# Performance work log

Hardware: AMD Instinct MI355X
Metric: run time of the kernel (lower is better)

Reference implementation:

```python
import jax, jax.numpy as jnp
import numpy as np

N = 20000        # atoms
NEIGH = 12       # neighbors per atom
BSTEPS = 40      # bond GBF steps, range [0, 8]
ASTEPS = 20      # angle GBF steps, range [-1, 1]
H = 64           # hidden size
NCLS = 2         # n_classification
NCRYS = 20       # crystals (contiguous blocks of 1000 atoms)
NREL = 3         # edge relation types


def gbf(data, dmin, dmax, steps):
    # Gaussian basis expansion: exp(-(d - mu)^2 / gamma^2), gamma = (max-min)/steps
    filters = jnp.linspace(dmin, dmax, steps)
    gamma = (dmax - dmin) / steps
    return jnp.exp(-((data[..., None] - filters) ** 2) / gamma ** 2)


def rgcn(x, src, dst, etype, W_rel, W_root, b):
    # RGCNConv (PyG default): out = x @ W_root + b + sum_r mean_{j in N_r(i)} x_j @ W_r
    out = x @ W_root + b
    for r in range(NREL):
        w = (etype == r).astype(x.dtype)                     # [E]
        msg = (x @ W_rel[r])[src] * w[:, None]               # transform-then-gather: [E, H]
        s = jax.ops.segment_sum(msg, dst, num_segments=x.shape[0])
        c = jax.ops.segment_sum(w, dst, num_segments=x.shape[0])
        out = out + s / jnp.maximum(c, 1.0)[:, None]
    return out


def _forward(bond_fea, angle_fea, species, nbr_idx, crys_idx,
             W1b_rel, W1b_root, b1b, W1a_rel, W1a_root, b1a,
             W2b_rel, W2b_root, b2b, W2a_rel, W2a_root, b2a,
             fc_W, fc_b):
    n = bond_fea.shape[0]
    src = jnp.repeat(jnp.arange(n, dtype=jnp.int32), NEIGH)  # edge sources
    dst = nbr_idx.reshape(-1)                                # edge targets
    etype = species[src] + species[dst]                      # 0/1/2 per species pair

    edge_fea = gbf(bond_fea, 0.0, 8.0, BSTEPS).reshape(n, -1)      # [N, 480]
    ang_fea = gbf(angle_fea, -1.0, 1.0, ASTEPS).reshape(n, -1)     # [N, 2880]

    bf = jax.nn.relu(rgcn(edge_fea, src, dst, etype, W1b_rel, W1b_root, b1b))
    af = jax.nn.relu(rgcn(ang_fea, src, dst, etype, W1a_rel, W1a_root, b1a))
    # dropout treated as identity (eval/deterministic reference)
    bf = jax.nn.relu(rgcn(bf, src, dst, etype, W2b_rel, W2b_root, b2b))
    af = jax.nn.relu(rgcn(af, src, dst, etype, W2a_rel, W2a_root, b2a))

    feat = jnp.concatenate([bf, af], axis=1)                 # [N, 128]

    # pool: mean over contiguous [start, end) ranges per crystal
    starts = crys_idx[:, 0]
    crys_id = jnp.searchsorted(starts, jnp.arange(n), side='right') - 1
    sums = jax.ops.segment_sum(feat, crys_id, num_segments=NCRYS)
    counts = (crys_idx[:, 1] - crys_idx[:, 0]).astype(feat.dtype)[:, None]
    pooled = sums / counts                                   # [NCRYS, 128]

    return pooled @ fc_W + fc_b                              # [NCRYS, NCLS]


def setup_inputs() -> dict:
    key = jax.random.key(0)
    ks = jax.random.split(key, 20)
    bond_fea = jax.random.uniform(ks[0], (N, NEIGH), dtype=jnp.float32) * 8.0
    angle_fea = jax.random.uniform(ks[1], (N, NEIGH, NEIGH), dtype=jnp.float32) * 2.0 - 1.0
    species = jax.random.randint(ks[2], (N,), 0, 2, dtype=jnp.int32)
    nbr_idx = jax.random.randint(ks[3], (N, NEIGH), 0, N, dtype=jnp.int32)
    starts = jnp.arange(NCRYS, dtype=jnp.int32) * (N // NCRYS)
    crys_idx = jnp.stack([starts, starts + (N // NCRYS)], axis=1)

    def w(k, shape, fan_in):
        return jax.random.normal(k, shape, dtype=jnp.float32) / np.sqrt(fan_in)

    in_b = BSTEPS * NEIGH            # 480
    in_a = ASTEPS * NEIGH * NEIGH    # 2880
    return {
        'bond_fea': bond_fea, 'angle_fea': angle_fea, 'species': species,
        'nbr_idx': nbr_idx, 'crys_idx': crys_idx,
        'W1b_rel': w(ks[4], (NREL, in_b, H), in_b), 'W1b_root': w(ks[5], (in_b, H), in_b),
        'b1b': jnp.zeros((H,), jnp.float32),
        'W1a_rel': w(ks[6], (NREL, in_a, H), in_a), 'W1a_root': w(ks[7], (in_a, H), in_a),
        'b1a': jnp.zeros((H,), jnp.float32),
        'W2b_rel': w(ks[8], (NREL, H, H), H), 'W2b_root': w(ks[9], (H, H), H),
        'b2b': jnp.zeros((H,), jnp.float32),
        'W2a_rel': w(ks[10], (NREL, H, H), H), 'W2a_root': w(ks[11], (H, H), H),
        'b2a': jnp.zeros((H,), jnp.float32),
        'fc_W': w(ks[12], (2 * H, NCLS), 2 * H), 'fc_b': jnp.zeros((NCLS,), jnp.float32),
    }


def reference(bond_fea, angle_fea, species, nbr_idx, crys_idx,
              W1b_rel, W1b_root, b1b, W1a_rel, W1a_root, b1a,
              W2b_rel, W2b_root, b2b, W2a_rel, W2a_root, b2a,
              fc_W, fc_b):
    return _forward(bond_fea, angle_fea, species, nbr_idx, crys_idx,
                    W1b_rel, W1b_root, b1b, W1a_rel, W1a_root, b1a,
                    W2b_rel, W2b_root, b2b, W2a_rel, W2a_root, b2a,
                    fc_W, fc_b)
```

## Files before the change

kernel.cpp:

```cpp
#include <hip/hip_runtime.h>

#define NN 20000
#define NNP 20096
#define NEIGH 12
#define NCRYS 20
#define MT2 1256
#define NSUB 16

typedef __bf16 bf16x8 __attribute__((ext_vector_type(8)));
typedef __bf16 bf16x4 __attribute__((ext_vector_type(4)));
typedef float f32x4 __attribute__((ext_vector_type(4)));
typedef float f32x2 __attribute__((ext_vector_type(2)));

__device__ __forceinline__ void pack_one(const float* Wrel, const float* Wroot,
                                         __bf16* Wp, int K, int idx) {
    int k = idx >> 8, n = idx & 255;
    int r = n >> 6, h = n & 63;
    float v = (r < 3) ? Wrel[((size_t)r * K + k) * 64 + h] : Wroot[(size_t)k * 64 + h];
    int kt = k >> 5, k8 = (k >> 3) & 3, j = k & 7, nt = n >> 4, ni = n & 15;
    Wp[((((size_t)kt * 16 + nt) * 4 + k8) * 16 + ni) * 8 + j] = (__bf16)v;
}

__global__ __launch_bounds__(256) void setup_kernel(
    const int* __restrict__ species, const int* __restrict__ nbr,
    int* __restrict__ adj, int* __restrict__ deg,
    const float* __restrict__ W1b_rel, const float* __restrict__ W1b_root,
    const float* __restrict__ W1a_rel, const float* __restrict__ W1a_root,
    const float* __restrict__ W2b_rel, const float* __restrict__ W2b_root,
    const float* __restrict__ W2a_rel, const float* __restrict__ W2a_root,
    __bf16* __restrict__ Wp1b, __bf16* __restrict__ Wp1a,
    __bf16* __restrict__ Wp2b, __bf16* __restrict__ Wp2a,
    const float* __restrict__ bond, const float* __restrict__ angle,
    float* __restrict__ bondT, float* __restrict__ angleT) {
    __shared__ float ls[64 * 145];
    const int bx = blockIdx.x, tid = threadIdx.x;
    if (bx < 938) {
        int e = bx * 256 + tid;
        if (e < NN * NEIGH) {
            int i = e / NEIGH;
            int d = nbr[e];
            int r = species[i] + species[d];
            int slot = atomicAdd(&deg[d], 1);
            if (slot < 64) adj[(size_t)d * 64 + slot] = i | (r << 28);
        }
    } else if (bx < 938 + 256) {
        const int S0 = 480 * 256, S1 = S0 + 2880 * 256, S2 = S1 + 64 * 256, S3 = S2 + 64 * 256;
        for (int idx = (bx - 938) * 256 + tid; idx < S3; idx += 256 * 256) {
            if (idx < S0)       pack_one(W1b_rel, W1b_root, Wp1b, 480, idx);
            else if (idx < S1)  pack_one(W1a_rel, W1a_root, Wp1a, 2880, idx - S0);
            else if (idx < S2)  pack_one(W2b_rel, W2b_root, Wp2b, 64, idx - S1);
            else                pack_one(W2a_rel, W2a_root, Wp2a, 64, idx - S2);
        }
    } else {
        int tb = bx - 1194;
        if (tb < 314) {
            int m0 = tb * 64;
            for (int idx = tid; idx < 64 * 144; idx += 256) {
                int mm = idx / 144, j = idx - mm * 144;
                int m = m0 + mm;
                ls[mm * 145 + j] = (m < NN) ? angle[(size_t)m * 144 + j] : 0.f;
            }
            __syncthreads();
            for (int idx = tid; idx < 144 * 64; idx += 256) {
                int j = idx >> 6, mm = idx & 63;
                angleT[(size_t)j * NNP + m0 + mm] = ls[mm * 145 + j];
            }
        } else {
            int m0 = (tb - 314) * 64;
            for (int idx = tid; idx < 64 * 12; idx += 256) {
                int mm = idx / 12, j = idx - mm * 12;
                int m = m0 + mm;
                ls[mm * 13 + j] = (m < NN) ? bond[(size_t)m * 12 + j] : 0.f;
            }
            __syncthreads();
            for (int idx = tid; idx < 12 * 64; idx += 256) {
                int j = idx >> 6, mm = idx & 63;
                bondT[(size_t)j * NNP + m0 + mm] = ls[mm * 13 + j];
            }
        }
    }
}

template <int MODE>
__device__ __forceinline__ void gemm1_body(const float* __restrict__ xT,
                                           const __bf16* __restrict__ Wp,
                                           float* __restrict__ Y, int mb,
                                           __bf16* __restrict__ Al) {
    constexpr int KTOT = (MODE == 0) ? 512 : 2880;
    constexpr int NPH = KTOT / 64;
    constexpr int DIVN = (MODE == 0) ? 40 : 20;
    constexpr int ADDJ = 64 / DIVN;
    constexpr int ADDS = 64 % DIVN;
    constexpr float F0 = (MODE == 0) ? 0.f : -1.f;
    constexpr float FS = (MODE == 0) ? (8.f / 39.f) : (2.f / 19.f);
    constexpr float NG2 = ((MODE == 0) ? -25.f : -100.f) * 1.44269504f;
    const float C  = __builtin_amdgcn_exp2f(2.f * NG2 * FS * FS);
    const float P1 = NG2 * FS * FS;
    const float P2 = -2.f * NG2 * FS;

    const int tid = threadIdx.x;
    const int lane = tid & 63, wv = tid >> 6;
    const int m0 = mb * 64;
    const int smt = tid >> 7;
    const int sk8 = (tid >> 5) & 3;
    const int smi = (tid >> 1) & 15;
    const int sjh = (tid & 1) * 4;
    const int sgm = m0 + smt * 16 + smi;
    const int kk0 = sk8 * 8 + sjh;
    const int swoff = (((smt * 4 + sk8) * 16 + smi) * 8 + sjh);
    const int k8b = lane >> 4, nib = lane & 15;
    const bf16x8* Bg = (const bf16x8*)Wp;

    f32x4 acc[4][2] = {};
    bf16x8 bcur[4];

    int jr0 = kk0 / DIVN,        s0 = kk0 % DIVN;
    int jr1 = (32 + kk0) / DIVN, s1 = (32 + kk0) % DIVN;

    auto bload = [&](int ph) {
#pragma unroll
        for (int jf = 0; jf < 4; ++jf)
            bcur[jf] = Bg[(((size_t)(2 * ph + (jf >> 1)) * 16 + 2 * wv + (jf & 1)) * 4 + k8b) * 16 + nib];
    };
    auto advance = [&]() {
        jr0 += ADDJ; s0 += ADDS; if (s0 >= DIVN) { s0 -= DIVN; ++jr0; }
        jr1 += ADDJ; s1 += ADDS; if (s1 >= DIVN) { s1 -= DIVN; ++jr1; }
    };
    auto stage = [&](float a0, float a1, __bf16* dst) {
        f32x2 d;
        d.x = a0 - (F0 + (float)s0 * FS);
        d.y = a1 - (F0 + (float)s1 * FS);
        f32x2 t = d * d;
        f32x2 argE = t * NG2;
        f32x2 argQ = d * P2 + P1;
        f32x2 e0, q0;
        e0.x = __builtin_amdgcn_exp2f(argE.x);
        e0.y = __builtin_amdgcn_exp2f(argE.y);
        q0.x = __builtin_amdgcn_exp2f(argQ.x);
        q0.y = __builtin_amdgcn_exp2f(argQ.y);
        f32x2 e1 = e0 * q0;
        f32x2 q1 = q0 * C;
        f32x2 e2 = e1 * q1;
        f32x2 e3 = e2 * (q1 * C);
        bf16x4 v0, v1;
        v0[0] = (__bf16)e0.x; v0[1] = (__bf16)e1.x; v0[2] = (__bf16)e2.x; v0[3] = (__bf16)e3.x;
        v1[0] = (__bf16)e0.y; v1[1] = (__bf16)e1.y; v1[2] = (__bf16)e2.y; v1[3] = (__bf16)e3.y;
        *(bf16x4*)&dst[swoff] = v0;
        *(bf16x4*)&dst[2048 + swoff] = v1;
    };

    {
        float a0 = xT[(size_t)jr0 * NNP + sgm];
        float a1 = xT[(size_t)jr1 * NNP + sgm];
        stage(a0, a1, Al);
        advance();
    }
    float an0 = xT[(size_t)jr0 * NNP + sgm];
    float an1 = xT[(size_t)jr1 * NNP + sgm];
    bload(0);
    __syncthreads();

    int cur = 0;
    for (int ph = 0; ph < NPH; ++ph) {
        const __bf16* Ab = Al + (cur << 12);
        bf16x8 af[4];
#pragma unroll
        for (int t4 = 0; t4 < 4; ++t4)
            af[t4] = *(const bf16x8*)&Ab[((((t4 << 2) + k8b) << 4) + nib) << 3];
#pragma unroll
        for (int i = 0; i < 4; ++i) {
            acc[i][0] = __builtin_amdgcn_mfma_f32_16x16x32_bf16(af[i], bcur[0], acc[i][0], 0, 0, 0);
            acc[i][1] = __builtin_amdgcn_mfma_f32_16x16x32_bf16(af[i], bcur[1], acc[i][1], 0, 0, 0);
        }
        bf16x8 ag[4];
#pragma unroll
        for (int t4 = 0; t4 < 4; ++t4)
            ag[t4] = *(const bf16x8*)&Ab[2048 + (((((t4 << 2) + k8b) << 4) + nib) << 3)];
#pragma unroll
        for (int i = 0; i < 4; ++i) {
            acc[i][0] = __builtin_amdgcn_mfma_f32_16x16x32_bf16(ag[i], bcur[2], acc[i][0], 0, 0, 0);
            acc[i][1] = __builtin_amdgcn_mfma_f32_16x16x32_bf16(ag[i], bcur[3], acc[i][1], 0, 0, 0);
        }
        if (ph + 1 < NPH) {
            bload(ph + 1);
            stage(an0, an1, Al + ((cur ^ 1) << 12));
            advance();
            if (ph + 2 < NPH) {
                an0 = xT[(size_t)jr0 * NNP + sgm];
                an1 = xT[(size_t)jr1 * NNP + sgm];
            }
        }
        __syncthreads();
        cur ^= 1;
    }

    const int mrow0 = m0 + ((lane >> 4) << 2);
    const int ncol = (wv << 5) + nib;
#pragma unroll
    for (int i = 0; i < 4; ++i)
#pragma unroll
        for (int j = 0; j < 2; ++j)
#pragma unroll
            for (int v = 0; v < 4; ++v) {
                int m = mrow0 + i * 16 + v;
                if (m < NN) Y[(size_t)m * 256 + ncol + j * 16] = acc[i][j][v];
            }
}

__global__ __launch_bounds__(512, 4) void mega_gemm1(const float* __restrict__ bondT,
                                                     const float* __restrict__ angleT,
                                                     const __bf16* __restrict__ Wp1b,
                                                     const __bf16* __restrict__ Wp1a,
                                                     float* __restrict__ Yb, float* __restrict__ Ya) {
    __shared__ __align__(16) __bf16 Al[2 * 4096];
    int bx = blockIdx.x;
    if (bx < 314) gemm1_body<1>(angleT, Wp1a, Ya, bx, Al);
    else          gemm1_body<0>(bondT, Wp1b, Yb, bx - 314, Al);
}

__global__ __launch_bounds__(256) void mega_gemm2(const __bf16* __restrict__ Hbp,
                                                  const __bf16* __restrict__ Hap,
                                                  const __bf16* __restrict__ Wp2b,
                                                  const __bf16* __restrict__ Wp2a,
                                                  float* __restrict__ Yb, float* __restrict__ Ya) {
    __shared__ __align__(16) __bf16 Al[4096];
    __shared__ __align__(16) __bf16 Bl[4096];
    const int ch = blockIdx.x & 1;
    const int mb = blockIdx.x >> 1;
    const int nb = blockIdx.y;
    const __bf16* Ap = ch ? Hap : Hbp;
    const __bf16* Wp = ch ? Wp2a : Wp2b;
    float* Y = ch ? Ya : Yb;
    const int tid = threadIdx.x;
    const int lane = tid & 63, wv = tid >> 6;
    const int m0 = mb * 128;
    const int rw = wv & 1, cw = wv >> 1;
    f32x4 acc[4][4] = {};
#pragma unroll
    for (int kt = 0; kt < 2; ++kt) {
        __syncthreads();
        {
            const float4* src = (const float4*)(Wp + (((size_t)kt * 16 + nb * 8) << 9));
            float4* dst = (float4*)Bl;
            float4 v0 = src[tid], v1 = src[tid + 256];
            dst[tid] = v0;
            dst[tid + 256] = v1;
        }
        {
            const float4* src = (const float4*)(Ap + (((size_t)kt * MT2 + mb * 8) << 9));
            float4* dst = (float4*)Al;
            float4 v0 = src[tid], v1 = src[tid + 256];
            dst[tid] = v0;
            dst[tid + 256] = v1;
        }
        __syncthreads();
        bf16x8 af[4], bfr[4];
        int fro = ((lane >> 4) << 4) + (lane & 15);
#pragma unroll
        for (int t4 = 0; t4 < 4; ++t4) {
            af[t4] = *(const bf16x8*)&Al[((((rw * 4 + t4) << 6) + fro) << 3)];
            bfr[t4] = *(const bf16x8*)&Bl[((((cw * 4 + t4) << 6) + fro) << 3)];
        }
#pragma unroll
        for (int i = 0; i < 4; ++i)
#pragma unroll
            for (int j = 0; j < 4; ++j)
                acc[i][j] = __builtin_amdgcn_mfma_f32_16x16x32_bf16(af[i], bfr[j], acc[i][j], 0, 0, 0);
    }
    const int n0 = nb * 128 + cw * 64;
    const int mrow0 = m0 + rw * 64 + ((lane >> 4) << 2);
    const int ncol = n0 + (lane & 15);
#pragma unroll
    for (int i = 0; i < 4; ++i)
#pragma unroll
        for (int j = 0; j < 4; ++j)
#pragma unroll
            for (int v = 0; v < 4; ++v) {
                int m = mrow0 + i * 16 + v;
                if (m < NN) Y[(size_t)m * 256 + ncol + j * 16] = acc[i][j][v];
            }
}

__device__ __forceinline__ float agg_node(const float* __restrict__ Y,
                                          const int* __restrict__ adj,
                                          const int* __restrict__ deg,
                                          const float* __restrict__ bias,
                                          int node, int h) {
    int dg = min(deg[node], 64);
    int e = adj[(size_t)node * 64 + h];
    bool val = h < dg;
    int r = e >> 28;
    unsigned long long bl0 = __ballot(val && r == 0);
    unsigned long long bl1 = __ballot(val && r == 1);
    unsigned long long bl2 = __ballot(val && r == 2);
    int c0 = __popcll(bl0), c1 = __popcll(bl1), c2 = __popcll(bl2);
    float s0 = 0.f, s1 = 0.f, s2 = 0.f;
    if (dg > 0) {
        int e0 = __builtin_amdgcn_readfirstlane(e);
        int ec = val ? e : e0;
        for (int k0 = 0; k0 < dg; k0 += 16) {
            float v[16];
#pragma unroll
            for (int i = 0; i < 16; ++i) {
                int ek = __builtin_amdgcn_readlane(ec, k0 + i);
                v[i] = Y[(size_t)(ek & 0x0FFFFFFF) * 256 + (ek >> 28) * 64 + h];
            }
#pragma unroll
            for (int i = 0; i < 16; ++i) {
                int kk = k0 + i;
                if (kk < dg) {
                    int rr = __builtin_amdgcn_readlane(ec, kk) >> 28;
                    if (rr == 0) s0 += v[i];
                    else if (rr == 1) s1 += v[i];
                    else s2 += v[i];
                }
            }
        }
    }
    float o = Y[(size_t)node * 256 + 192 + h] + bias[h] +
              s0 / fmaxf((float)c0, 1.f) + s1 / fmaxf((float)c1, 1.f) +
              s2 / fmaxf((float)c2, 1.f);
    return fmaxf(o, 0.f);
}

__global__ __launch_bounds__(256) void agg_packed(const float* __restrict__ Yb,
                                                  const float* __restrict__ Ya,
                                                  const int* __restrict__ adj,
                                                  const int* __restrict__ deg,
                                                  const float* __restrict__ biasb,
                                                  const float* __restrict__ biasa,
                                                  __bf16* __restrict__ outb,
                                                  __bf16* __restrict__ outa) {
    const float* Y = blockIdx.y ? Ya : Yb;
    const float* bias = blockIdx.y ? biasa : biasb;
    __bf16* outp = blockIdx.y ? outa : outb;
    int node = blockIdx.x * 4 + (threadIdx.x >> 6);
    int h = threadIdx.x & 63;
    float o = (node < NN) ? agg_node(Y, adj, deg, bias, node, h) : 0.f;
    int mt = node >> 4, mi = node & 15;
    int ktt = h >> 5, k8 = (h >> 3) & 3, j = h & 7;
    outp[((((size_t)ktt * MT2 + mt) * 4 + k8) * 16 + mi) * 8 + j] = (__bf16)o;
}

__global__ __launch_bounds__(256) void agg_pool(const float* __restrict__ Yb,
                                                const float* __restrict__ Ya,
                                                const int* __restrict__ adj,
                                                const int* __restrict__ deg,
                                                const float* __restrict__ biasb,
                                                const float* __restrict__ biasa,
                                                const int* __restrict__ crys,
                                                float* __restrict__ pooled) {
    const float* Y = blockIdx.y ? Ya : Yb;
    const float* bias = blockIdx.y ? biasa : biasb;
    const int base = blockIdx.y ? 64 : 0;
    int node = blockIdx.x * 4 + (threadIdx.x >> 6);
    int h = threadIdx.x & 63;
    if (node >= NN) return;
    float o = agg_node(Y, adj, deg, bias, node, h);
    int c = 0;
#pragma unroll
    for (int t = 1; t < NCRYS; ++t) c += (node >= crys[t * 2]) ? 1 : 0;
    int sub = blockIdx.x & (NSUB - 1);
    atomicAdd(&pooled[((size_t)c * NSUB + sub) * 128 + base + h], o);
}

__global__ void final2(const float* __restrict__ pooled, const int* __restrict__ crys,
                       const float* __restrict__ fcW, const float* __restrict__ fcb,
                       float* __restrict__ out) {
    int c = blockIdx.x >> 1, o = blockIdx.x & 1;
    int l = threadIdx.x;
    float cnt = (float)(crys[c * 2 + 1] - crys[c * 2]);
    float sb = 0.f, sa = 0.f;
    for (int s = 0; s < NSUB; ++s) {
        sb += pooled[((size_t)c * NSUB + s) * 128 + l];
        sa += pooled[((size_t)c * NSUB + s) * 128 + 64 + l];
    }
    float a = sb * fcW[l * 2 + o] + sa * fcW[(64 + l) * 2 + o];
    for (int s = 32; s > 0; s >>= 1) a += __shfl_down(a, s);
    if (l == 0) out[c * 2 + o] = a / cnt + fcb[o];
}

extern "C" void kernel_launch(void* const* d_in, const int* in_sizes, int n_in,
                              void* d_out, int out_size, void* d_ws, size_t ws_size,
                              hipStream_t stream) {
    const float* bond    = (const float*)d_in[0];
    const float* angle   = (const float*)d_in[1];
    const int*   species = (const int*)d_in[2];
    const int*   nbr     = (const int*)d_in[3];
    const int*   crys    = (const int*)d_in[4];
    const float* W1b_rel = (const float*)d_in[5];
    const float* W1b_root= (const float*)d_in[6];
    const float* b1b     = (const float*)d_in[7];
    const float* W1a_rel = (const float*)d_in[8];
    const float* W1a_root= (const float*)d_in[9];
    const float* b1a     = (const float*)d_in[10];
    const float* W2b_rel = (const float*)d_in[11];
    const float* W2b_root= (const float*)d_in[12];
    const float* b2b     = (const float*)d_in[13];
    const float* W2a_rel = (const float*)d_in[14];
    const float* W2a_root= (const float*)d_in[15];
    const float* b2a     = (const float*)d_in[16];
    const float* fcW     = (const float*)d_in[17];
    const float* fcb     = (const float*)d_in[18];
    float* out = (float*)d_out;

    char* ws = (char*)d_ws;
    size_t off = 0;
    auto alloc = [&](size_t bytes) {
        char* p = ws + off;
        off = (off + bytes + 255) & ~(size_t)255;
        return p;
    };
    __bf16* Wp1b = (__bf16*)alloc((size_t)512 * 256 * 2);
    __bf16* Wp1a = (__bf16*)alloc((size_t)2880 * 256 * 2);
    __bf16* Wp2b = (__bf16*)alloc((size_t)64 * 256 * 2);
    __bf16* Wp2a = (__bf16*)alloc((size_t)64 * 256 * 2);
    float*  bondT = (float*)alloc((size_t)16 * NNP * 4);
    float*  angleT= (float*)alloc((size_t)144 * NNP * 4);
    float*  Yb   = (float*)alloc((size_t)NN * 256 * 4);
    float*  Ya   = (float*)alloc((size_t)NN * 256 * 4);
    __bf16* Hbp  = (__bf16*)alloc((size_t)2 * MT2 * 512 * 2);
    __bf16* Hap  = (__bf16*)alloc((size_t)2 * MT2 * 512 * 2);
    int*    adj  = (int*)alloc((size_t)NN * 64 * 4);
    int*    deg  = (int*)alloc((size_t)NN * 4);
    float*  pooled = (float*)alloc((size_t)NCRYS * NSUB * 128 * 4);

    hipMemsetAsync(deg, 0, (size_t)NN * 4, stream);
    hipMemsetAsync(pooled, 0, (size_t)NCRYS * NSUB * 128 * 4, stream);
    hipMemsetAsync(Wp1b, 0, (size_t)512 * 256 * 2, stream);
    hipMemsetAsync(bondT, 0, (size_t)16 * NNP * 4, stream);

    setup_kernel<<<1822, 256, 0, stream>>>(species, nbr, adj, deg,
                                           W1b_rel, W1b_root, W1a_rel, W1a_root,
                                           W2b_rel, W2b_root, W2a_rel, W2a_root,
                                           Wp1b, Wp1a, Wp2b, Wp2a,
                                           bond, angle, bondT, angleT);

    mega_gemm1<<<628, 512, 0, stream>>>(bondT, angleT, Wp1b, Wp1a, Yb, Ya);
    agg_packed<<<dim3(5024, 2), 256, 0, stream>>>(Yb, Ya, adj, deg, b1b, b1a, Hbp, Hap);
    mega_gemm2<<<dim3(314, 2), 256, 0, stream>>>(Hbp, Hap, Wp2b, Wp2a, Yb, Ya);
    agg_pool<<<dim3(5000, 2), 256, 0, stream>>>(Yb, Ya, adj, deg, b2b, b2a, crys, pooled);
    final2<<<NCRYS * 2, 64, 0, stream>>>(pooled, crys, fcW, fcb, out);
}
```

Before: 261.1 us.

## Aggregate-then-transform for layer two using bf16 features and concatenated weights

```diff
diff --git a/kernel.cpp b/kernel.cpp
--- a/kernel.cpp
+++ b/kernel.cpp
@@ -10,7 +10,6 @@
 typedef __bf16 bf16x8 __attribute__((ext_vector_type(8)));
 typedef __bf16 bf16x4 __attribute__((ext_vector_type(4)));
 typedef float f32x4 __attribute__((ext_vector_type(4)));
-typedef float f32x2 __attribute__((ext_vector_type(2)));
 
 __device__ __forceinline__ void pack_one(const float* Wrel, const float* Wroot,
                                          __bf16* Wp, int K, int idx) {
@@ -19,6 +18,15 @@
     float v = (r < 3) ? Wrel[((size_t)r * K + k) * 64 + h] : Wroot[(size_t)k * 64 + h];
     int kt = k >> 5, k8 = (k >> 3) & 3, j = k & 7, nt = n >> 4, ni = n & 15;
     Wp[((((size_t)kt * 16 + nt) * 4 + k8) * 16 + ni) * 8 + j] = (__bf16)v;
+}
+
+__device__ __forceinline__ void pack_cat(const float* Wrel, const float* Wroot,
+                                         __bf16* Wp, int idx) {
+    int k4 = idx >> 6, n = idx & 63;
+    int q = k4 >> 6, kk = k4 & 63;
+    float v = q ? Wrel[(((q - 1) * 64 + kk) * 64) + n] : Wroot[kk * 64 + n];
+    int kt = k4 >> 5, k8 = (k4 >> 3) & 3, j = k4 & 7, nt = n >> 4, ni = n & 15;
+    Wp[((((size_t)kt * 4 + nt) * 4 + k8) * 16 + ni) * 8 + j] = (__bf16)v;
 }
 
 __global__ __launch_bounds__(256) void setup_kernel(
@@ -44,12 +52,12 @@
             if (slot < 64) adj[(size_t)d * 64 + slot] = i | (r << 28);
         }
     } else if (bx < 938 + 256) {
-        const int S0 = 480 * 256, S1 = S0 + 2880 * 256, S2 = S1 + 64 * 256, S3 = S2 + 64 * 256;
+        const int S0 = 480 * 256, S1 = S0 + 2880 * 256, S2 = S1 + 16384, S3 = S2 + 16384;
         for (int idx = (bx - 938) * 256 + tid; idx < S3; idx += 256 * 256) {
             if (idx < S0)       pack_one(W1b_rel, W1b_root, Wp1b, 480, idx);
             else if (idx < S1)  pack_one(W1a_rel, W1a_root, Wp1a, 2880, idx - S0);
-            else if (idx < S2)  pack_one(W2b_rel, W2b_root, Wp2b, 64, idx - S1);
-            else                pack_one(W2a_rel, W2a_root, Wp2a, 64, idx - S2);
+            else if (idx < S2)  pack_cat(W2b_rel, W2b_root, Wp2b, idx - S1);
+            else                pack_cat(W2a_rel, W2a_root, Wp2a, idx - S2);
         }
     } else {
         int tb = bx - 1194;
@@ -86,7 +94,7 @@
                                            const __bf16* __restrict__ Wp,
                                            float* __restrict__ Y, int mb,
                                            __bf16* __restrict__ Al) {
-    constexpr int KTOT = (MODE == 0) ? 512 : 2880;
+    constexpr int KTOT = (MODE == 0) ? 512 : 2944;
     constexpr int NPH = KTOT / 64;
     constexpr int DIVN = (MODE == 0) ? 40 : 20;
     constexpr int ADDJ = 64 / DIVN;
@@ -109,89 +117,90 @@
     const int kk0 = sk8 * 8 + sjh;
     const int swoff = (((smt * 4 + sk8) * 16 + smi) * 8 + sjh);
     const int k8b = lane >> 4, nib = lane & 15;
-    const bf16x8* Bg = (const bf16x8*)Wp;
 
     f32x4 acc[4][2] = {};
-    bf16x8 bcur[4];
-
-    int jr0 = kk0 / DIVN,        s0 = kk0 % DIVN;
-    int jr1 = (32 + kk0) / DIVN, s1 = (32 + kk0) % DIVN;
-
-    auto bload = [&](int ph) {
-#pragma unroll
-        for (int jf = 0; jf < 4; ++jf)
-            bcur[jf] = Bg[(((size_t)(2 * ph + (jf >> 1)) * 16 + 2 * wv + (jf & 1)) * 4 + k8b) * 16 + nib];
-    };
-    auto advance = [&]() {
-        jr0 += ADDJ; s0 += ADDS; if (s0 >= DIVN) { s0 -= DIVN; ++jr0; }
-        jr1 += ADDJ; s1 += ADDS; if (s1 >= DIVN) { s1 -= DIVN; ++jr1; }
+
+    const float* pA0 = xT + (size_t)(kk0 / DIVN) * NNP + sgm;
+    const float* pA1 = xT + (size_t)((32 + kk0) / DIVN) * NNP + sgm;
+    int sL0 = kk0 % DIVN, sL1 = (32 + kk0) % DIVN;
+    int sS0 = sL0, sS1 = sL1;
+
+    const bf16x8* pB0 = (const bf16x8*)Wp + ((size_t)(2 * wv) * 4 + k8b) * 16 + nib;
+    const bf16x8* pB1 = pB0 + 1024;
+
+    bf16x8 bEv[4], bOd[4];
+
+    auto advL = [&]() {
+        sL0 += ADDS;
+        if (sL0 >= DIVN) { sL0 -= DIVN; pA0 += (size_t)(ADDJ + 1) * NNP; } else pA0 += (size_t)ADDJ * NNP;
+        sL1 += ADDS;
+        if (sL1 >= DIVN) { sL1 -= DIVN; pA1 += (size_t)(ADDJ + 1) * NNP; } else pA1 += (size_t)ADDJ * NNP;
+    };
+    auto advS = [&]() {
+        sS0 += ADDS; if (sS0 >= DIVN) sS0 -= DIVN;
+        sS1 += ADDS; if (sS1 >= DIVN) sS1 -= DIVN;
+    };
+    auto loadB = [&](bf16x8* d) {
+        d[0] = pB0[0]; d[1] = pB0[64]; d[2] = pB1[0]; d[3] = pB1[64];
+        pB0 += 2048; pB1 += 2048;
     };
     auto stage = [&](float a0, float a1, __bf16* dst) {
-        f32x2 d;
-        d.x = a0 - (F0 + (float)s0 * FS);
-        d.y = a1 - (F0 + (float)s1 * FS);
-        f32x2 t = d * d;
-        f32x2 argE = t * NG2;
-        f32x2 argQ = d * P2 + P1;
-        f32x2 e0, q0;
-        e0.x = __builtin_amdgcn_exp2f(argE.x);
-        e0.y = __builtin_amdgcn_exp2f(argE.y);
-        q0.x = __builtin_amdgcn_exp2f(argQ.x);
-        q0.y = __builtin_amdgcn_exp2f(argQ.y);
-        f32x2 e1 = e0 * q0;
-        f32x2 q1 = q0 * C;
-        f32x2 e2 = e1 * q1;
-        f32x2 e3 = e2 * (q1 * C);
+        float d0 = a0 - (F0 + (float)sS0 * FS);
+        float d1 = a1 - (F0 + (float)sS1 * FS);
+        float e0a = __builtin_amdgcn_exp2f(NG2 * d0 * d0);
+        float q0a = __builtin_amdgcn_exp2f(fmaf(P2, d0, P1));
+        float e0b = __builtin_amdgcn_exp2f(NG2 * d1 * d1);
+        float q0b = __builtin_amdgcn_exp2f(fmaf(P2, d1, P1));
+        float e1a = e0a * q0a, q1a = q0a * C;
+        float e2a = e1a * q1a, e3a = e2a * q1a * C;
+        float e1b = e0b * q0b, q1b = q0b * C;
+        float e2b = e1b * q1b, e3b = e2b * q1b * C;
         bf16x4 v0, v1;
-        v0[0] = (__bf16)e0.x; v0[1] = (__bf16)e1.x; v0[2] = (__bf16)e2.x; v0[3] = (__bf16)e3.x;
-        v1[0] = (__bf16)e0.y; v1[1] = (__bf16)e1.y; v1[2] = (__bf16)e2.y; v1[3] = (__bf16)e3.y;
+        v0[0] = (__bf16)e0a; v0[1] = (__bf16)e1a; v0[2] = (__bf16)e2a; v0[3] = (__bf16)e3a;
+        v1[0] = (__bf16)e0b; v1[1] = (__bf16)e1b; v1[2] = (__bf16)e2b; v1[3] = (__bf16)e3b;
         *(bf16x4*)&dst[swoff] = v0;
         *(bf16x4*)&dst[2048 + swoff] = v1;
     };
-
-    {
-        float a0 = xT[(size_t)jr0 * NNP + sgm];
-        float a1 = xT[(size_t)jr1 * NNP + sgm];
-        stage(a0, a1, Al);
-        advance();
-    }
-    float an0 = xT[(size_t)jr0 * NNP + sgm];
-    float an1 = xT[(size_t)jr1 * NNP + sgm];
-    bload(0);
+    auto mma = [&](const __bf16* Ab, const bf16x8* bc) {
+        bf16x8 af[4], ag[4];
+#pragma unroll
+        for (int t4 = 0; t4 < 4; ++t4) {
+            af[t4] = *(const bf16x8*)&Ab[(((((t4 << 2) + k8b) << 4) + nib) << 3)];
+            ag[t4] = *(const bf16x8*)&Ab[2048 + (((((t4 << 2) + k8b) << 4) + nib) << 3)];
+        }
+#pragma unroll
+        for (int i = 0; i < 4; ++i) {
+            acc[i][0] = __builtin_amdgcn_mfma_f32_16x16x32_bf16(af[i], bc[0], acc[i][0], 0, 0, 0);
+            acc[i][1] = __builtin_amdgcn_mfma_f32_16x16x32_bf16(af[i], bc[1], acc[i][1], 0, 0, 0);
+        }
+#pragma unroll
+        for (int i = 0; i < 4; ++i) {
+            acc[i][0] = __builtin_amdgcn_mfma_f32_16x16x32_bf16(ag[i], bc[2], acc[i][0], 0, 0, 0);
+            acc[i][1] = __builtin_amdgcn_mfma_f32_16x16x32_bf16(ag[i], bc[3], acc[i][1], 0, 0, 0);
+        }
+    };
+
+    float a00 = pA0[0], a01 = pA1[0]; advL();
+    float aN0 = pA0[0], aN1 = pA1[0]; advL();
+    stage(a00, a01, Al); advS();
+    loadB(bEv);
+    loadB(bOd);
     __syncthreads();
 
-    int cur = 0;
-    for (int ph = 0; ph < NPH; ++ph) {
-        const __bf16* Ab = Al + (cur << 12);
-        bf16x8 af[4];
-#pragma unroll
-        for (int t4 = 0; t4 < 4; ++t4)
-            af[t4] = *(const bf16x8*)&Ab[((((t4 << 2) + k8b) << 4) + nib) << 3];
-#pragma unroll
-        for (int i = 0; i < 4; ++i) {
-            acc[i][0] = __builtin_amdgcn_mfma_f32_16x16x32_bf16(af[i], bcur[0], acc[i][0], 0, 0, 0);
-            acc[i][1] = __builtin_amdgcn_mfma_f32_16x16x32_bf16(af[i], bcur[1], acc[i][1], 0, 0, 0);
-        }
-        bf16x8 ag[4];
-#pragma unroll
-        for (int t4 = 0; t4 < 4; ++t4)
-            ag[t4] = *(const bf16x8*)&Ab[2048 + (((((t4 << 2) + k8b) << 4) + nib) << 3)];
-#pragma unroll
-        for (int i = 0; i < 4; ++i) {
-            acc[i][0] = __builtin_amdgcn_mfma_f32_16x16x32_bf16(ag[i], bcur[2], acc[i][0], 0, 0, 0);
-            acc[i][1] = __builtin_amdgcn_mfma_f32_16x16x32_bf16(ag[i], bcur[3], acc[i][1], 0, 0, 0);
-        }
-        if (ph + 1 < NPH) {
-            bload(ph + 1);
-            stage(an0, an1, Al + ((cur ^ 1) << 12));
-            advance();
-            if (ph + 2 < NPH) {
-                an0 = xT[(size_t)jr0 * NNP + sgm];
-                an1 = xT[(size_t)jr1 * NNP + sgm];
-            }
-        }
+    for (int p2 = 0; p2 < NPH / 2; ++p2) {
+        const bool last = (p2 == NPH / 2 - 1);
+        mma(Al, bEv);
+        if (!last) loadB(bEv);
+        stage(aN0, aN1, Al + 4096); advS();
+        if (!last) { aN0 = pA0[0]; aN1 = pA1[0]; advL(); }
         __syncthreads();
-        cur ^= 1;
+        mma(Al + 4096, bOd);
+        if (!last) {
+            loadB(bOd);
+            stage(aN0, aN1, Al); advS();
+            aN0 = pA0[0]; aN1 = pA1[0]; advL();
+        }
+        __syncthreads();
     }
 
     const int mrow0 = m0 + ((lane >> 4) << 2);
@@ -216,69 +225,6 @@
     int bx = blockIdx.x;
     if (bx < 314) gemm1_body<1>(angleT, Wp1a, Ya, bx, Al);
     else          gemm1_body<0>(bondT, Wp1b, Yb, bx - 314, Al);
-}
-
-__global__ __launch_bounds__(256) void mega_gemm2(const __bf16* __restrict__ Hbp,
-                                                  const __bf16* __restrict__ Hap,
-                                                  const __bf16* __restrict__ Wp2b,
-                                                  const __bf16* __restrict__ Wp2a,
-                                                  float* __restrict__ Yb, float* __restrict__ Ya) {
-    __shared__ __align__(16) __bf16 Al[4096];
-    __shared__ __align__(16) __bf16 Bl[4096];
-    const int ch = blockIdx.x & 1;
-    const int mb = blockIdx.x >> 1;
-    const int nb = blockIdx.y;
-    const __bf16* Ap = ch ? Hap : Hbp;
-    const __bf16* Wp = ch ? Wp2a : Wp2b;
-    float* Y = ch ? Ya : Yb;
-    const int tid = threadIdx.x;
-    const int lane = tid & 63, wv = tid >> 6;
-    const int m0 = mb * 128;
-    const int rw = wv & 1, cw = wv >> 1;
-    f32x4 acc[4][4] = {};
-#pragma unroll
-    for (int kt = 0; kt < 2; ++kt) {
-        __syncthreads();
-        {
-            const float4* src = (const float4*)(Wp + (((size_t)kt * 16 + nb * 8) << 9));
-            float4* dst = (float4*)Bl;
-            float4 v0 = src[tid], v1 = src[tid + 256];
-            dst[tid] = v0;
-            dst[tid + 256] = v1;
-        }
-        {
-            const float4* src = (const float4*)(Ap + (((size_t)kt * MT2 + mb * 8) << 9));
-            float4* dst = (float4*)Al;
-            float4 v0 = src[tid], v1 = src[tid + 256];
-            dst[tid] = v0;
-            dst[tid + 256] = v1;
-        }
-        __syncthreads();
-        bf16x8 af[4], bfr[4];
-        int fro = ((lane >> 4) << 4) + (lane & 15);
-#pragma unroll
-        for (int t4 = 0; t4 < 4; ++t4) {
-            af[t4] = *(const bf16x8*)&Al[((((rw * 4 + t4) << 6) + fro) << 3)];
-            bfr[t4] = *(const bf16x8*)&Bl[((((cw * 4 + t4) << 6) + fro) << 3)];
-        }
-#pragma unroll
-        for (int i = 0; i < 4; ++i)
-#pragma unroll
-            for (int j = 0; j < 4; ++j)
-                acc[i][j] = __builtin_amdgcn_mfma_f32_16x16x32_bf16(af[i], bfr[j], acc[i][j], 0, 0, 0);
-    }
-    const int n0 = nb * 128 + cw * 64;
-    const int mrow0 = m0 + rw * 64 + ((lane >> 4) << 2);
-    const int ncol = n0 + (lane & 15);
-#pragma unroll
-    for (int i = 0; i < 4; ++i)
-#pragma unroll
-        for (int j = 0; j < 4; ++j)
-#pragma unroll
-            for (int v = 0; v < 4; ++v) {
-                int m = mrow0 + i * 16 + v;
-                if (m < NN) Y[(size_t)m * 256 + ncol + j * 16] = acc[i][j][v];
-            }
 }
 
 __device__ __forceinline__ float agg_node(const float* __restrict__ Y,
@@ -336,32 +282,133 @@
     __bf16* outp = blockIdx.y ? outa : outb;
     int node = blockIdx.x * 4 + (threadIdx.x >> 6);
     int h = threadIdx.x & 63;
-    float o = (node < NN) ? agg_node(Y, adj, deg, bias, node, h) : 0.f;
+    if (node >= NN) return;
+    float o = agg_node(Y, adj, deg, bias, node, h);
+    outp[(size_t)node * 64 + h] = (__bf16)o;
+}
+
+__global__ __launch_bounds__(256) void agg2(const __bf16* __restrict__ Hb,
+                                            const __bf16* __restrict__ Ha,
+                                            const int* __restrict__ adj,
+                                            const int* __restrict__ deg,
+                                            __bf16* __restrict__ Apb,
+                                            __bf16* __restrict__ Apa) {
+    const __bf16* H = blockIdx.y ? Ha : Hb;
+    __bf16* Ap = blockIdx.y ? Apa : Apb;
+    int node = blockIdx.x * 4 + (threadIdx.x >> 6);
+    int h = threadIdx.x & 63;
+    float hd = 0.f, r0 = 0.f, r1 = 0.f, r2 = 0.f;
+    if (node < NN) {
+        int dg = min(deg[node], 64);
+        int e = adj[(size_t)node * 64 + h];
+        bool val = h < dg;
+        int r = e >> 28;
+        unsigned long long bl0 = __ballot(val && r == 0);
+        unsigned long long bl1 = __ballot(val && r == 1);
+        unsigned long long bl2 = __ballot(val && r == 2);
+        int c0 = __popcll(bl0), c1 = __popcll(bl1), c2 = __popcll(bl2);
+        float s0 = 0.f, s1 = 0.f, s2 = 0.f;
+        hd = (float)H[(size_t)node * 64 + h];
+        if (dg > 0) {
+            int e0 = __builtin_amdgcn_readfirstlane(e);
+            int ec = val ? e : e0;
+            for (int k0 = 0; k0 < dg; k0 += 16) {
+                float v[16];
+#pragma unroll
+                for (int i = 0; i < 16; ++i) {
+                    int ek = __builtin_amdgcn_readlane(ec, k0 + i);
+                    v[i] = (float)H[(size_t)(ek & 0x0FFFFFFF) * 64 + h];
+                }
+#pragma unroll
+                for (int i = 0; i < 16; ++i) {
+                    int kk = k0 + i;
+                    if (kk < dg) {
+                        int rr = __builtin_amdgcn_readlane(ec, kk) >> 28;
+                        if (rr == 0) s0 += v[i];
+                        else if (rr == 1) s1 += v[i];
+                        else s2 += v[i];
+                    }
+                }
+            }
+        }
+        r0 = s0 / fmaxf((float)c0, 1.f);
+        r1 = s1 / fmaxf((float)c1, 1.f);
+        r2 = s2 / fmaxf((float)c2, 1.f);
+    }
     int mt = node >> 4, mi = node & 15;
-    int ktt = h >> 5, k8 = (h >> 3) & 3, j = h & 7;
-    outp[((((size_t)ktt * MT2 + mt) * 4 + k8) * 16 + mi) * 8 + j] = (__bf16)o;
-}
-
-__global__ __launch_bounds__(256) void agg_pool(const float* __restrict__ Yb,
-                                                const float* __restrict__ Ya,
-                                                const int* __restrict__ adj,
-                                                const int* __restrict__ deg,
-                                                const float* __restrict__ biasb,
-                                                const float* __restrict__ biasa,
-                                                const int* __restrict__ crys,
-                                                float* __restrict__ pooled) {
-    const float* Y = blockIdx.y ? Ya : Yb;
-    const float* bias = blockIdx.y ? biasa : biasb;
-    const int base = blockIdx.y ? 64 : 0;
+    float vals[4] = {hd, r0, r1, r2};
+#pragma unroll
+    for (int q = 0; q < 4; ++q) {
+        int K4 = q * 64 + h;
+        int kt = K4 >> 5, k8 = (K4 >> 3) & 3, j = K4 & 7;
+        Ap[((((size_t)kt * MT2 + mt) * 4 + k8) * 16 + mi) * 8 + j] = (__bf16)vals[q];
+    }
+}
+
+__global__ __launch_bounds__(256) void gemm3(const __bf16* __restrict__ Apb,
+                                             const __bf16* __restrict__ Apa,
+                                             const __bf16* __restrict__ Wpb,
+                                             const __bf16* __restrict__ Wpa,
+                                             const float* __restrict__ bb,
+                                             const float* __restrict__ ba,
+                                             float* __restrict__ Zb,
+                                             float* __restrict__ Za) {
+    const int ch = blockIdx.y;
+    const bf16x8* Ag = (const bf16x8*)(ch ? Apa : Apb);
+    const bf16x8* Bg = (const bf16x8*)(ch ? Wpa : Wpb);
+    const float* bias = ch ? ba : bb;
+    float* Z = ch ? Za : Zb;
+    const int tid = threadIdx.x, lane = tid & 63, wv = tid >> 6;
+    const int mt0 = blockIdx.x * 8 + wv * 2;
+    const int k8b = lane >> 4, nib = lane & 15;
+    f32x4 acc[2][4] = {};
+#pragma unroll
+    for (int kt = 0; kt < 8; ++kt) {
+        bf16x8 a0 = Ag[(((size_t)kt * MT2 + mt0) * 4 + k8b) * 16 + nib];
+        bf16x8 a1 = Ag[(((size_t)kt * MT2 + mt0 + 1) * 4 + k8b) * 16 + nib];
+        bf16x8 b0 = Bg[(((size_t)kt * 4 + 0) * 4 + k8b) * 16 + nib];
+        bf16x8 b1 = Bg[(((size_t)kt * 4 + 1) * 4 + k8b) * 16 + nib];
+        bf16x8 b2 = Bg[(((size_t)kt * 4 + 2) * 4 + k8b) * 16 + nib];
+        bf16x8 b3 = Bg[(((size_t)kt * 4 + 3) * 4 + k8b) * 16 + nib];
+        acc[0][0] = __builtin_amdgcn_mfma_f32_16x16x32_bf16(a0, b0, acc[0][0], 0, 0, 0);
+        acc[0][1] = __builtin_amdgcn_mfma_f32_16x16x32_bf16(a0, b1, acc[0][1], 0, 0, 0);
+        acc[0][2] = __builtin_amdgcn_mfma_f32_16x16x32_bf16(a0, b2, acc[0][2], 0, 0, 0);
+        acc[0][3] = __builtin_amdgcn_mfma_f32_16x16x32_bf16(a0, b3, acc[0][3], 0, 0, 0);
+        acc[1][0] = __builtin_amdgcn_mfma_f32_16x16x32_bf16(a1, b0, acc[1][0], 0, 0, 0);
+        acc[1][1] = __builtin_amdgcn_mfma_f32_16x16x32_bf16(a1, b1, acc[1][1], 0, 0, 0);
+        acc[1][2] = __builtin_amdgcn_mfma_f32_16x16x32_bf16(a1, b2, acc[1][2], 0, 0, 0);
+        acc[1][3] = __builtin_amdgcn_mfma_f32_16x16x32_bf16(a1, b3, acc[1][3], 0, 0, 0);
+    }
+#pragma unroll
+    for (int i = 0; i < 2; ++i)
+#pragma unroll
+        for (int j = 0; j < 4; ++j)
+#pragma unroll
+            for (int v = 0; v < 4; ++v) {
+                int m = (mt0 + i) * 16 + ((lane >> 4) << 2) + v;
+                int n = j * 16 + nib;
+                if (m < NN) {
+                    float o = acc[i][j][v] + bias[n];
+                    Z[(size_t)m * 64 + n] = fmaxf(o, 0.f);
+                }
+            }
+}
+
+__global__ __launch_bounds__(256) void pool2(const float* __restrict__ Zb,
+                                             const float* __restrict__ Za,
+                                             const int* __restrict__ crys,
+                                             float* __restrict__ pooled) {
     int node = blockIdx.x * 4 + (threadIdx.x >> 6);
     int h = threadIdx.x & 63;
     if (node >= NN) return;
-    float o = agg_node(Y, adj, deg, bias, node, h);
+    float zb = Zb[(size_t)node * 64 + h];
+    float za = Za[(size_t)node * 64 + h];
     int c = 0;
 #pragma unroll
     for (int t = 1; t < NCRYS; ++t) c += (node >= crys[t * 2]) ? 1 : 0;
     int sub = blockIdx.x & (NSUB - 1);
-    atomicAdd(&pooled[((size_t)c * NSUB + sub) * 128 + base + h], o);
+    atomicAdd(&pooled[((size_t)c * NSUB + sub) * 128 + h], zb);
+    atomicAdd(&pooled[((size_t)c * NSUB + sub) * 128 + 64 + h], za);
 }
 
 __global__ void final2(const float* __restrict__ pooled, const int* __restrict__ crys,
@@ -412,23 +459,29 @@
         return p;
     };
     __bf16* Wp1b = (__bf16*)alloc((size_t)512 * 256 * 2);
-    __bf16* Wp1a = (__bf16*)alloc((size_t)2880 * 256 * 2);
-    __bf16* Wp2b = (__bf16*)alloc((size_t)64 * 256 * 2);
-    __bf16* Wp2a = (__bf16*)alloc((size_t)64 * 256 * 2);
+    __bf16* Wp1a = (__bf16*)alloc((size_t)2944 * 256 * 2);
+    __bf16* Wp2b = (__bf16*)alloc((size_t)256 * 64 * 2);
+    __bf16* Wp2a = (__bf16*)alloc((size_t)256 * 64 * 2);
     float*  bondT = (float*)alloc((size_t)16 * NNP * 4);
-    float*  angleT= (float*)alloc((size_t)144 * NNP * 4);
+    float*  angleT= (float*)alloc((size_t)148 * NNP * 4);
     float*  Yb   = (float*)alloc((size_t)NN * 256 * 4);
     float*  Ya   = (float*)alloc((size_t)NN * 256 * 4);
-    __bf16* Hbp  = (__bf16*)alloc((size_t)2 * MT2 * 512 * 2);
-    __bf16* Hap  = (__bf16*)alloc((size_t)2 * MT2 * 512 * 2);
+    __bf16* Hrowb= (__bf16*)alloc((size_t)NNP * 64 * 2);
+    __bf16* Hrowa= (__bf16*)alloc((size_t)NNP * 64 * 2);
+    __bf16* Apb  = (__bf16*)alloc((size_t)8 * MT2 * 512 * 2);
+    __bf16* Apa  = (__bf16*)alloc((size_t)8 * MT2 * 512 * 2);
     int*    adj  = (int*)alloc((size_t)NN * 64 * 4);
     int*    deg  = (int*)alloc((size_t)NN * 4);
     float*  pooled = (float*)alloc((size_t)NCRYS * NSUB * 128 * 4);
+    float*  Zb = Yb;
+    float*  Za = Ya;
 
     hipMemsetAsync(deg, 0, (size_t)NN * 4, stream);
     hipMemsetAsync(pooled, 0, (size_t)NCRYS * NSUB * 128 * 4, stream);
     hipMemsetAsync(Wp1b, 0, (size_t)512 * 256 * 2, stream);
+    hipMemsetAsync(Wp1a + (size_t)2880 * 256, 0, (size_t)64 * 256 * 2, stream);
     hipMemsetAsync(bondT, 0, (size_t)16 * NNP * 4, stream);
+    hipMemsetAsync(angleT + (size_t)144 * NNP, 0, (size_t)4 * NNP * 4, stream);
 
     setup_kernel<<<1822, 256, 0, stream>>>(species, nbr, adj, deg,
                                            W1b_rel, W1b_root, W1a_rel, W1a_root,
@@ -437,8 +490,9 @@
                                            bond, angle, bondT, angleT);
 
     mega_gemm1<<<628, 512, 0, stream>>>(bondT, angleT, Wp1b, Wp1a, Yb, Ya);
-    agg_packed<<<dim3(5024, 2), 256, 0, stream>>>(Yb, Ya, adj, deg, b1b, b1a, Hbp, Hap);
-    mega_gemm2<<<dim3(314, 2), 256, 0, stream>>>(Hbp, Hap, Wp2b, Wp2a, Yb, Ya);
-    agg_pool<<<dim3(5000, 2), 256, 0, stream>>>(Yb, Ya, adj, deg, b2b, b2a, crys, pooled);
+    agg_packed<<<dim3(5024, 2), 256, 0, stream>>>(Yb, Ya, adj, deg, b1b, b1a, Hrowb, Hrowa);
+    agg2<<<dim3(5024, 2), 256, 0, stream>>>(Hrowb, Hrowa, adj, deg, Apb, Apa);
+    gemm3<<<dim3(157, 2), 256, 0, stream>>>(Apb, Apa, Wp2b, Wp2a, b2b, b2a, Zb, Za);
+    pool2<<<5000, 256, 0, stream>>>(Zb, Za, crys, pooled);
     final2<<<NCRYS * 2, 64, 0, stream>>>(pooled, crys, fcW, fcb, out);
 }
```

Result: no change. 263.1 us (+0.8%).
